# Optimization experiments

Measured on AMD Instinct MI355X. Metric: run time of the kernel, lower is better.

## Reference

```python
import jax, jax.numpy as jnp
import numpy as np

B, C_IN, H, W = 4, 256, 64, 64
LATENT = 256


def conv1x1(x, w, b):
    # x: [B, Cin, H, W], w: [Cout, Cin], b: [Cout]
    return jnp.einsum('bchw,oc->bohw', x, w) + b[None, :, None, None]


def setup_inputs() -> dict:
    key = jax.random.key(0)
    ks = jax.random.split(key, 9)
    s_in = 1.0 / np.sqrt(C_IN)
    s_lat = 1.0 / np.sqrt(LATENT)
    return {
        'x': jax.random.normal(ks[0], (B, C_IN, H, W), dtype=jnp.float32),
        'Wq': jax.random.normal(ks[1], (LATENT, C_IN), dtype=jnp.float32) * s_in,
        'bq': jax.random.normal(ks[2], (LATENT,), dtype=jnp.float32) * 0.01,
        'Wk': jax.random.normal(ks[3], (LATENT, C_IN), dtype=jnp.float32) * s_in,
        'bk': jax.random.normal(ks[4], (LATENT,), dtype=jnp.float32) * 0.01,
        'Wv': jax.random.normal(ks[5], (LATENT, C_IN), dtype=jnp.float32) * s_in,
        'bv': jax.random.normal(ks[6], (LATENT,), dtype=jnp.float32) * 0.01,
        'Wo': jax.random.normal(ks[7], (C_IN, LATENT), dtype=jnp.float32) * s_lat,
        'bo': jax.random.normal(ks[8], (C_IN,), dtype=jnp.float32) * 0.01,
    }


def reference(x, Wq, bq, Wk, bk, Wv, bv, Wo, bo):
    b, _, h, w = x.shape
    n = h * w
    q = conv1x1(x, Wq, bq).reshape(b, LATENT, n)  # [B, L, N]
    k = conv1x1(x, Wk, bk).reshape(b, LATENT, n)
    v = conv1x1(x, Wv, bv).reshape(b, LATENT, n)
    scale = jnp.sqrt(jnp.asarray(LATENT, dtype=x.dtype))
    # attention[b, i, j] = sum_c q[b, c, i] * k[b, c, j]
    attn = jnp.einsum('bci,bcj->bij', q, k) / scale
    # faithful to original: softmax over dim=1 (query index i, per column j)
    attn = jax.nn.softmax(attn, axis=1)
    # res[b, c, j] = sum_i v[b, c, i] * attn[b, i, j]
    res = jnp.einsum('bci,bij->bcj', v, attn).reshape(b, LATENT, h, w)
    return conv1x1(res, Wo, bo)
```

## Files before the change

### kernel.cpp

```cpp
#include <hip/hip_runtime.h>

#define B_  4
#define C_  256
#define N_  4096
#define SCALE 0.0625f

typedef short s8v __attribute__((ext_vector_type(8)));
typedef float f4v __attribute__((ext_vector_type(4)));

static __device__ __forceinline__ ushort f2bf(float f) {
  union { float f; uint u; } v; v.f = f;
  return (ushort)((v.u + 0x7FFFu + ((v.u >> 16) & 1u)) >> 16);
}

static __device__ __forceinline__ void gload_lds16(const ushort* g, ushort* l) {
  __builtin_amdgcn_global_load_lds(
      (const __attribute__((address_space(1))) void*)g,
      (__attribute__((address_space(3))) void*)l, 16, 0, 0);
}

__global__ __launch_bounds__(256) void xpose_cast(
    const float* __restrict__ x, ushort* __restrict__ x_t,
    float* __restrict__ den)
{
  const int b  = blockIdx.z;
  const int c0 = blockIdx.y * 64;
  const int n0 = blockIdx.x * 64;
  __shared__ float t[64][65];

  if (blockIdx.y == 0 && threadIdx.x < 64)
    den[b * N_ + n0 + threadIdx.x] = 0.f;

  const int tc = threadIdx.x >> 4;
  const int tn = (threadIdx.x & 15) * 4;
  #pragma unroll
  for (int cc = 0; cc < 64; cc += 16) {
    float4 v = *(const float4*)(x + (size_t)(b * C_ + c0 + cc + tc) * N_ + n0 + tn);
    t[cc + tc][tn + 0] = v.x;
    t[cc + tc][tn + 1] = v.y;
    t[cc + tc][tn + 2] = v.z;
    t[cc + tc][tn + 3] = v.w;
  }
  __syncthreads();

  const int on = threadIdx.x >> 2;
  const int oc = (threadIdx.x & 3) * 16;
  union { ushort us[16]; uint4 q[2]; } o;
  #pragma unroll
  for (int i = 0; i < 16; ++i) o.us[i] = f2bf(t[oc + i][on]);
  ushort* dst = x_t + (size_t)(b * N_ + n0 + on) * C_ + c0 + oc;
  *(uint4*)dst       = o.q[0];
  *(uint4*)(dst + 8) = o.q[1];
}

__global__ __launch_bounds__(256, 2) void qkv_mfma(
    const ushort* __restrict__ x_t,
    const float* __restrict__ Wq, const float* __restrict__ bq,
    const float* __restrict__ Wk, const float* __restrict__ bk,
    const float* __restrict__ Wv, const float* __restrict__ bv,
    ushort* __restrict__ q_t, ushort* __restrict__ k_t, ushort* __restrict__ v_bf)
{
  const int p = blockIdx.z >> 2;
  const int b = blockIdx.z & 3;
  const float* W  = (p == 0) ? Wq : (p == 1) ? Wk : Wv;
  const float* bi = (p == 0) ? bq : (p == 1) ? bk : bv;
  const int l0    = blockIdx.y * 64;
  const int nseg  = blockIdx.x * 512;

  const int tid  = threadIdx.x;
  const int lane = tid & 63;
  const int wave = tid >> 6;
  const int l16  = lane & 15;
  const int quad = lane >> 4;

  __shared__ __align__(16) ushort w_lds[64 * 264];
  __shared__ __align__(16) ushort x_lds[64 * 264];

  for (int g = tid; g < 4096; g += 256) {
    int row = g >> 6, col4 = (g & 63) * 4;
    float4 wv = *(const float4*)(W + (size_t)(l0 + row) * 256 + col4);
    *(ushort4*)&w_lds[row * 264 + col4] =
        make_ushort4(f2bf(wv.x), f2bf(wv.y), f2bf(wv.z), f2bf(wv.w));
  }
  __syncthreads();

  s8v kw[4][8];
  #pragma unroll
  for (int lt = 0; lt < 4; ++lt)
    #pragma unroll
    for (int cs = 0; cs < 8; ++cs)
      kw[lt][cs] = *(const s8v*)&w_lds[(lt * 16 + l16) * 264 + quad * 8 + cs * 32];

  float bias_l[4];
  #pragma unroll
  for (int lt = 0; lt < 4; ++lt) bias_l[lt] = bi[l0 + lt * 16 + l16];

  for (int it = 0; it < 8; ++it) {
    const int n0 = nseg + it * 64;
    {
      const ushort* xseg = x_t + (size_t)(b * N_ + n0) * C_;
      #pragma unroll
      for (int k = 0; k < 8; ++k) {
        int c = tid + k * 256;
        uint4 d = *(const uint4*)(xseg + (size_t)c * 8);
        *(uint4*)&x_lds[(c >> 5) * 264 + (c & 31) * 8] = d;
      }
    }
    __syncthreads();

    f4v s[4];
    #pragma unroll
    for (int lt = 0; lt < 4; ++lt) s[lt] = (f4v){0.f, 0.f, 0.f, 0.f};
    const ushort* xa_base = x_lds + (wave * 16 + l16) * 264 + quad * 8;
    #pragma unroll
    for (int cs = 0; cs < 8; ++cs) {
      s8v xa = *(const s8v*)(xa_base + cs * 32);
      #pragma unroll
      for (int lt = 0; lt < 4; ++lt)
        s[lt] = __builtin_amdgcn_mfma_f32_16x16x32_bf16(xa, kw[lt][cs], s[lt], 0, 0, 0);
    }

    const int nb = n0 + wave * 16 + quad * 4;
    if (p < 2) {
      ushort* outp = (p == 0) ? q_t : k_t;
      #pragma unroll
      for (int lt = 0; lt < 4; ++lt) {
        const int l = l0 + lt * 16 + l16;
        #pragma unroll
        for (int r = 0; r < 4; ++r)
          outp[(size_t)(b * N_ + nb + r) * C_ + l] = f2bf(s[lt][r] + bias_l[lt]);
      }
    } else {
      #pragma unroll
      for (int lt = 0; lt < 4; ++lt) {
        const int c_out = l0 + lt * 16 + l16;
        *(ushort4*)&v_bf[(size_t)(b * C_ + c_out) * N_ + nb] =
            make_ushort4(f2bf(s[lt][0] + bias_l[lt]), f2bf(s[lt][1] + bias_l[lt]),
                         f2bf(s[lt][2] + bias_l[lt]), f2bf(s[lt][3] + bias_l[lt]));
      }
    }
    __syncthreads();
  }
}

__global__ __launch_bounds__(256, 2) void flash8b(
    const ushort* __restrict__ q_t, const ushort* __restrict__ k_t,
    const ushort* __restrict__ v_bf, ushort* __restrict__ res0,
    ushort* __restrict__ res1, float* __restrict__ den)
{
  const int tid  = threadIdx.x;
  const int lane = tid & 63;
  const int wave = tid >> 6;
  const int l16  = lane & 15;
  const int quad = lane >> 4;
  const int jw    = blockIdx.x * 64;
  const int seg   = blockIdx.y;
  const int ibase = seg * 2048;
  const int b     = blockIdx.z;

  const int wqk_j = wave & 1;
  const int wqk_i = wave >> 1;

  __shared__ __align__(16) ushort q_lds[64 * 256];
  __shared__ __align__(16) ushort p_lds[64 * 64];

  s8v kf[2][8];
  #pragma unroll
  for (int jt = 0; jt < 2; ++jt) {
    const ushort* kp = k_t + (size_t)(b * N_ + jw + wqk_j * 32 + jt * 16 + l16) * C_ + quad * 8;
    #pragma unroll
    for (int cs = 0; cs < 8; ++cs) kf[jt][cs] = *(const s8v*)(kp + cs * 32);
  }

  f4v acc[4][4];
  #pragma unroll
  for (int m = 0; m < 4; ++m)
    #pragma unroll
    for (int t = 0; t < 4; ++t) acc[m][t] = (f4v){0.f, 0.f, 0.f, 0.f};
  float dacc0 = 0.f, dacc1 = 0.f;

  const ushort* vbase0 = v_bf + (size_t)(b * C_ + wave * 64 + l16) * N_ + quad * 8;

  for (int it = 0; it < 32; ++it) {
    const int i0 = ibase + it * 64;

    {
      const ushort* qseg = q_t + ((size_t)(b * N_) + i0) * C_;
      const int plo = lane & 31;
      #pragma unroll
      for (int k = 0; k < 8; ++k) {
        const int row = k * 8 + wave * 2 + (lane >> 5);
        const ushort* src = qseg + row * 256 + ((plo ^ (row & 7)) << 3);
        gload_lds16(src, &q_lds[k * 2048 + wave * 512]);
      }
    }

    s8v av[4][2];
    #pragma unroll
    for (int m = 0; m < 4; ++m)
      #pragma unroll
      for (int ks = 0; ks < 2; ++ks)
        av[m][ks] = *(const s8v*)(vbase0 + (size_t)(m * 16) * N_ + i0 + ks * 32);

    __syncthreads();

    #pragma unroll
    for (int itile = 0; itile < 2; ++itile) {
      const int i_loc = (wqk_i * 2 + itile) * 16;
      f4v s0 = (f4v){0.f, 0.f, 0.f, 0.f};
      f4v s1 = (f4v){0.f, 0.f, 0.f, 0.f};
      const int qrow = i_loc + l16;
      const ushort* qa_row = q_lds + qrow * 256;
      const int qsw = qrow & 7;
      __builtin_amdgcn_s_setprio(1);
      #pragma unroll
      for (int cs = 0; cs < 8; ++cs) {
        s8v qa = *(const s8v*)(qa_row + (((quad + 4 * cs) ^ qsw) << 3));
        s0 = __builtin_amdgcn_mfma_f32_16x16x32_bf16(qa, kf[0][cs], s0, 0, 0, 0);
        s1 = __builtin_amdgcn_mfma_f32_16x16x32_bf16(qa, kf[1][cs], s1, 0, 0, 0);
      }
      __builtin_amdgcn_s_setprio(0);
      {
        float e0 = __expf(s0[0] * SCALE), e1 = __expf(s0[1] * SCALE);
        float e2 = __expf(s0[2] * SCALE), e3 = __expf(s0[3] * SCALE);
        dacc0 += (e0 + e1) + (e2 + e3);
        const int row = wqk_j * 32 + l16;
        const int col = i_loc + quad * 4;
        *(ushort4*)&p_lds[row * 64 + ((((col >> 3) ^ (row & 7)) << 3) | (col & 7))] =
            make_ushort4(f2bf(e0), f2bf(e1), f2bf(e2), f2bf(e3));
      }
      {
        float e0 = __expf(s1[0] * SCALE), e1 = __expf(s1[1] * SCALE);
        float e2 = __expf(s1[2] * SCALE), e3 = __expf(s1[3] * SCALE);
        dacc1 += (e0 + e1) + (e2 + e3);
        const int row = wqk_j * 32 + 16 + l16;
        const int col = i_loc + quad * 4;
        *(ushort4*)&p_lds[row * 64 + ((((col >> 3) ^ (row & 7)) << 3) | (col & 7))] =
            make_ushort4(f2bf(e0), f2bf(e1), f2bf(e2), f2bf(e3));
      }
    }

    __syncthreads();

    #pragma unroll
    for (int ks = 0; ks < 2; ++ks) {
      s8v pb[4];
      #pragma unroll
      for (int t = 0; t < 4; ++t) {
        const int row = t * 16 + l16;
        const int col = ks * 32 + quad * 8;
        pb[t] = *(const s8v*)&p_lds[row * 64 + (((col >> 3) ^ (row & 7)) << 3)];
      }
      __builtin_amdgcn_s_setprio(1);
      #pragma unroll
      for (int m = 0; m < 4; ++m)
        #pragma unroll
        for (int t = 0; t < 4; ++t)
          acc[m][t] = __builtin_amdgcn_mfma_f32_16x16x32_bf16(av[m][ks], pb[t], acc[m][t], 0, 0, 0);
      __builtin_amdgcn_s_setprio(0);
    }
  }

  dacc0 += __shfl_xor(dacc0, 16);  dacc0 += __shfl_xor(dacc0, 32);
  dacc1 += __shfl_xor(dacc1, 16);  dacc1 += __shfl_xor(dacc1, 32);
  if (lane < 16) {
    atomicAdd(&den[b * N_ + jw + wqk_j * 32 + lane], dacc0);
    atomicAdd(&den[b * N_ + jw + wqk_j * 32 + 16 + lane], dacc1);
  }

  #pragma unroll
  for (int m = 0; m < 4; ++m) {
    const int c0 = wave * 64 + m * 16 + quad * 4;
    #pragma unroll
    for (int t = 0; t < 4; ++t) {
      const int row = t * 16 + l16;
      *(ushort4*)&q_lds[row * 256 + ((((c0 >> 3) ^ (row & 7)) << 3) | (c0 & 7))] =
          make_ushort4(f2bf(acc[m][t][0]), f2bf(acc[m][t][1]),
                       f2bf(acc[m][t][2]), f2bf(acc[m][t][3]));
    }
  }
  __syncthreads();
  {
    ushort* rp = (seg ? res1 : res0) + (size_t)(b * N_ + jw) * C_;
    #pragma unroll
    for (int k = 0; k < 8; ++k) {
      int c = tid + k * 256;
      int row = c >> 5, ch = c & 31;
      uint4 d = *(const uint4*)&q_lds[row * 256 + ((ch ^ (row & 7)) << 3)];
      *(uint4*)&rp[(size_t)row * C_ + ch * 8] = d;
    }
  }
}

__global__ __launch_bounds__(256, 2) void out_mfma(
    const ushort* __restrict__ res0, const ushort* __restrict__ res1,
    const float* __restrict__ Wo, const float* __restrict__ bo,
    const float* __restrict__ den, float* __restrict__ out)
{
  const int b    = blockIdx.z;
  const int co0  = blockIdx.y * 64;
  const int nseg = blockIdx.x * 128;

  const int tid  = threadIdx.x;
  const int lane = tid & 63;
  const int wave = tid >> 6;
  const int l16  = lane & 15;
  const int quad = lane >> 4;

  __shared__ __align__(16) ushort r_lds[2][64 * 264];

  for (int g = tid; g < 4096; g += 256) {
    int row = g >> 6, col4 = (g & 63) * 4;
    float4 wv = *(const float4*)(Wo + (size_t)(co0 + row) * 256 + col4);
    *(ushort4*)&r_lds[0][row * 264 + col4] =
        make_ushort4(f2bf(wv.x), f2bf(wv.y), f2bf(wv.z), f2bf(wv.w));
  }
  __syncthreads();

  s8v kw[4][8];
  #pragma unroll
  for (int lt = 0; lt < 4; ++lt)
    #pragma unroll
    for (int cs = 0; cs < 8; ++cs)
      kw[lt][cs] = *(const s8v*)&r_lds[0][(lt * 16 + l16) * 264 + quad * 8 + cs * 32];

  float bias_l[4];
  #pragma unroll
  for (int lt = 0; lt < 4; ++lt) bias_l[lt] = bo[co0 + lt * 16 + l16];

  __syncthreads();

  for (int it = 0; it < 2; ++it) {
    const int n0 = nseg + it * 64;
    {
      const ushort* r0 = res0 + (size_t)(b * N_ + n0) * C_;
      const ushort* r1 = res1 + (size_t)(b * N_ + n0) * C_;
      #pragma unroll
      for (int k = 0; k < 8; ++k) {
        int c = tid + k * 256;
        uint4 d0 = *(const uint4*)(r0 + (size_t)c * 8);
        uint4 d1 = *(const uint4*)(r1 + (size_t)c * 8);
        *(uint4*)&r_lds[0][(c >> 5) * 264 + (c & 31) * 8] = d0;
        *(uint4*)&r_lds[1][(c >> 5) * 264 + (c & 31) * 8] = d1;
      }
    }
    __syncthreads();

    f4v s[4];
    #pragma unroll
    for (int lt = 0; lt < 4; ++lt) s[lt] = (f4v){0.f, 0.f, 0.f, 0.f};
    #pragma unroll
    for (int buf = 0; buf < 2; ++buf) {
      const ushort* ra_base = r_lds[buf] + (wave * 16 + l16) * 264 + quad * 8;
      #pragma unroll
      for (int cs = 0; cs < 8; ++cs) {
        s8v ra = *(const s8v*)(ra_base + cs * 32);
        #pragma unroll
        for (int lt = 0; lt < 4; ++lt)
          s[lt] = __builtin_amdgcn_mfma_f32_16x16x32_bf16(ra, kw[lt][cs], s[lt], 0, 0, 0);
      }
    }

    const int nb = n0 + wave * 16 + quad * 4;
    float4 dv = *(const float4*)(den + (size_t)b * N_ + nb);
    const float di0 = 1.0f / dv.x, di1 = 1.0f / dv.y, di2 = 1.0f / dv.z, di3 = 1.0f / dv.w;
    #pragma unroll
    for (int lt = 0; lt < 4; ++lt) {
      const int co = co0 + lt * 16 + l16;
      *(float4*)&out[(size_t)(b * C_ + co) * N_ + nb] =
          make_float4(s[lt][0] * di0 + bias_l[lt], s[lt][1] * di1 + bias_l[lt],
                      s[lt][2] * di2 + bias_l[lt], s[lt][3] * di3 + bias_l[lt]);
    }
    __syncthreads();
  }
}

extern "C" void kernel_launch(void* const* d_in, const int* in_sizes, int n_in,
                              void* d_out, int out_size, void* d_ws, size_t ws_size,
                              hipStream_t stream)
{
  const float* x  = (const float*)d_in[0];
  const float* Wq = (const float*)d_in[1];
  const float* bq = (const float*)d_in[2];
  const float* Wk = (const float*)d_in[3];
  const float* bk = (const float*)d_in[4];
  const float* Wv = (const float*)d_in[5];
  const float* bv = (const float*)d_in[6];
  const float* Wo = (const float*)d_in[7];
  const float* bo = (const float*)d_in[8];
  float* out = (float*)d_out;

  char* ws = (char*)d_ws;
  ushort* q_t  = (ushort*)(ws);
  ushort* k_t  = (ushort*)(ws + (size_t)8  * 1024 * 1024);
  ushort* v_bf = (ushort*)(ws + (size_t)16 * 1024 * 1024);
  ushort* res0 = (ushort*)(ws + (size_t)24 * 1024 * 1024);
  ushort* res1 = (ushort*)(ws + (size_t)32 * 1024 * 1024);
  float*  den  = (float*) (ws + (size_t)40 * 1024 * 1024);
  ushort* x_t  = (ushort*)(ws + (size_t)40 * 1024 * 1024 + 65536);

  xpose_cast<<<dim3(64, 4, 4), dim3(256), 0, stream>>>(x, x_t, den);
  qkv_mfma <<<dim3(8, 4, 12),  dim3(256), 0, stream>>>(x_t, Wq, bq, Wk, bk, Wv, bv, q_t, k_t, v_bf);
  flash8b  <<<dim3(64, 2, 4),  dim3(256), 0, stream>>>(q_t, k_t, v_bf, res0, res1, den);
  out_mfma <<<dim3(32, 4, 4),  dim3(256), 0, stream>>>(res0, res1, Wo, bo, den, out);
}
```

Baseline: 203.6 us.

## Fuse Q/K/V projections into one kernel sharing each x tile

The QKV projection kernel now computes all three projections per block, so each loaded x tile is reused for Q, K and V instead of being read three times by separate blocks. Weights are loaded straight from global memory into registers, skipping the LDS staging. The x tile is loaded with direct global-to-LDS transfers using an XOR swizzle to avoid bank conflicts. The grid becomes 32x4x4 with two iterations per block. Holding three sets of weight fragments uses many more registers (96 s8v values), which risks spills or lower occupancy.

```diff
diff --git a/kernel.cpp b/kernel.cpp
--- a/kernel.cpp
+++ b/kernel.cpp
@@ -11,6 +11,15 @@
 static __device__ __forceinline__ ushort f2bf(float f) {
   union { float f; uint u; } v; v.f = f;
   return (ushort)((v.u + 0x7FFFu + ((v.u >> 16) & 1u)) >> 16);
+}
+
+static __device__ __forceinline__ s8v pack8(float4 a, float4 b) {
+  s8v r;
+  r[0] = (short)f2bf(a.x); r[1] = (short)f2bf(a.y);
+  r[2] = (short)f2bf(a.z); r[3] = (short)f2bf(a.w);
+  r[4] = (short)f2bf(b.x); r[5] = (short)f2bf(b.y);
+  r[6] = (short)f2bf(b.z); r[7] = (short)f2bf(b.w);
+  return r;
 }
 
 static __device__ __forceinline__ void gload_lds16(const ushort* g, ushort* l) {
@@ -53,19 +62,16 @@
   *(uint4*)(dst + 8) = o.q[1];
 }
 
-__global__ __launch_bounds__(256, 2) void qkv_mfma(
+__global__ __launch_bounds__(256, 2) void qkv3(
     const ushort* __restrict__ x_t,
     const float* __restrict__ Wq, const float* __restrict__ bq,
     const float* __restrict__ Wk, const float* __restrict__ bk,
     const float* __restrict__ Wv, const float* __restrict__ bv,
     ushort* __restrict__ q_t, ushort* __restrict__ k_t, ushort* __restrict__ v_bf)
 {
-  const int p = blockIdx.z >> 2;
-  const int b = blockIdx.z & 3;
-  const float* W  = (p == 0) ? Wq : (p == 1) ? Wk : Wv;
-  const float* bi = (p == 0) ? bq : (p == 1) ? bk : bv;
+  const int b     = blockIdx.z;
   const int l0    = blockIdx.y * 64;
-  const int nseg  = blockIdx.x * 512;
+  const int nseg  = blockIdx.x * 128;
 
   const int tid  = threadIdx.x;
   const int lane = tid & 63;
@@ -73,71 +79,82 @@
   const int l16  = lane & 15;
   const int quad = lane >> 4;
 
-  __shared__ __align__(16) ushort w_lds[64 * 264];
-  __shared__ __align__(16) ushort x_lds[64 * 264];
-
-  for (int g = tid; g < 4096; g += 256) {
-    int row = g >> 6, col4 = (g & 63) * 4;
-    float4 wv = *(const float4*)(W + (size_t)(l0 + row) * 256 + col4);
-    *(ushort4*)&w_lds[row * 264 + col4] =
-        make_ushort4(f2bf(wv.x), f2bf(wv.y), f2bf(wv.z), f2bf(wv.w));
-  }
-  __syncthreads();
-
-  s8v kw[4][8];
-  #pragma unroll
-  for (int lt = 0; lt < 4; ++lt)
-    #pragma unroll
-    for (int cs = 0; cs < 8; ++cs)
-      kw[lt][cs] = *(const s8v*)&w_lds[(lt * 16 + l16) * 264 + quad * 8 + cs * 32];
-
-  float bias_l[4];
-  #pragma unroll
-  for (int lt = 0; lt < 4; ++lt) bias_l[lt] = bi[l0 + lt * 16 + l16];
-
-  for (int it = 0; it < 8; ++it) {
+  __shared__ __align__(16) ushort x_lds[64 * 256];
+
+  const float* Ws[3] = {Wq, Wk, Wv};
+  const float* bs[3] = {bq, bk, bv};
+
+  s8v   kw[3][4][8];
+  float bias_l[3][4];
+  #pragma unroll
+  for (int p = 0; p < 3; ++p) {
+    #pragma unroll
+    for (int lt = 0; lt < 4; ++lt) {
+      const int row = l0 + lt * 16 + l16;
+      const float* wrow = Ws[p] + (size_t)row * 256 + quad * 8;
+      bias_l[p][lt] = bs[p][row];
+      #pragma unroll
+      for (int cs = 0; cs < 8; ++cs) {
+        float4 a  = *(const float4*)(wrow + cs * 32);
+        float4 c2 = *(const float4*)(wrow + cs * 32 + 4);
+        kw[p][lt][cs] = pack8(a, c2);
+      }
+    }
+  }
+
+  const int plo = lane & 31;
+
+  for (int it = 0; it < 2; ++it) {
     const int n0 = nseg + it * 64;
+
     {
       const ushort* xseg = x_t + (size_t)(b * N_ + n0) * C_;
       #pragma unroll
       for (int k = 0; k < 8; ++k) {
-        int c = tid + k * 256;
-        uint4 d = *(const uint4*)(xseg + (size_t)c * 8);
-        *(uint4*)&x_lds[(c >> 5) * 264 + (c & 31) * 8] = d;
-      }
-    }
-    __syncthreads();
-
-    f4v s[4];
-    #pragma unroll
-    for (int lt = 0; lt < 4; ++lt) s[lt] = (f4v){0.f, 0.f, 0.f, 0.f};
-    const ushort* xa_base = x_lds + (wave * 16 + l16) * 264 + quad * 8;
+        const int row = k * 8 + wave * 2 + (lane >> 5);
+        gload_lds16(xseg + row * 256 + ((plo ^ (row & 7)) << 3),
+                    &x_lds[k * 2048 + wave * 512]);
+      }
+    }
+    __syncthreads();
+
+    f4v s[3][4];
+    #pragma unroll
+    for (int p = 0; p < 3; ++p)
+      #pragma unroll
+      for (int lt = 0; lt < 4; ++lt) s[p][lt] = (f4v){0.f, 0.f, 0.f, 0.f};
+
+    const int qrow = wave * 16 + l16;
+    const ushort* xa_row = x_lds + qrow * 256;
+    const int qsw = qrow & 7;
     #pragma unroll
     for (int cs = 0; cs < 8; ++cs) {
-      s8v xa = *(const s8v*)(xa_base + cs * 32);
-      #pragma unroll
-      for (int lt = 0; lt < 4; ++lt)
-        s[lt] = __builtin_amdgcn_mfma_f32_16x16x32_bf16(xa, kw[lt][cs], s[lt], 0, 0, 0);
+      s8v xa = *(const s8v*)(xa_row + (((quad + 4 * cs) ^ qsw) << 3));
+      #pragma unroll
+      for (int p = 0; p < 3; ++p)
+        #pragma unroll
+        for (int lt = 0; lt < 4; ++lt)
+          s[p][lt] = __builtin_amdgcn_mfma_f32_16x16x32_bf16(xa, kw[p][lt][cs], s[p][lt], 0, 0, 0);
     }
 
     const int nb = n0 + wave * 16 + quad * 4;
-    if (p < 2) {
+    #pragma unroll
+    for (int p = 0; p < 2; ++p) {
       ushort* outp = (p == 0) ? q_t : k_t;
       #pragma unroll
       for (int lt = 0; lt < 4; ++lt) {
         const int l = l0 + lt * 16 + l16;
         #pragma unroll
         for (int r = 0; r < 4; ++r)
-          outp[(size_t)(b * N_ + nb + r) * C_ + l] = f2bf(s[lt][r] + bias_l[lt]);
-      }
-    } else {
-      #pragma unroll
-      for (int lt = 0; lt < 4; ++lt) {
-        const int c_out = l0 + lt * 16 + l16;
-        *(ushort4*)&v_bf[(size_t)(b * C_ + c_out) * N_ + nb] =
-            make_ushort4(f2bf(s[lt][0] + bias_l[lt]), f2bf(s[lt][1] + bias_l[lt]),
-                         f2bf(s[lt][2] + bias_l[lt]), f2bf(s[lt][3] + bias_l[lt]));
-      }
+          outp[(size_t)(b * N_ + nb + r) * C_ + l] = f2bf(s[p][lt][r] + bias_l[p][lt]);
+      }
+    }
+    #pragma unroll
+    for (int lt = 0; lt < 4; ++lt) {
+      const int c_out = l0 + lt * 16 + l16;
+      *(ushort4*)&v_bf[(size_t)(b * C_ + c_out) * N_ + nb] =
+          make_ushort4(f2bf(s[2][lt][0] + bias_l[2][lt]), f2bf(s[2][lt][1] + bias_l[2][lt]),
+                       f2bf(s[2][lt][2] + bias_l[2][lt]), f2bf(s[2][lt][3] + bias_l[2][lt]));
     }
     __syncthreads();
   }
@@ -400,7 +417,7 @@
   ushort* x_t  = (ushort*)(ws + (size_t)40 * 1024 * 1024 + 65536);
 
   xpose_cast<<<dim3(64, 4, 4), dim3(256), 0, stream>>>(x, x_t, den);
-  qkv_mfma <<<dim3(8, 4, 12),  dim3(256), 0, stream>>>(x_t, Wq, bq, Wk, bk, Wv, bv, q_t, k_t, v_bf);
+  qkv3     <<<dim3(32, 4, 4),  dim3(256), 0, stream>>>(x_t, Wq, bq, Wk, bk, Wv, bv, q_t, k_t, v_bf);
   flash8b  <<<dim3(64, 2, 4),  dim3(256), 0, stream>>>(q_t, k_t, v_bf, res0, res1, den);
   out_mfma <<<dim3(32, 4, 4),  dim3(256), 0, stream>>>(res0, res1, Wo, bo, den, out);
 }
```

Measured after the change: 538.8 us. 2.65x slower.
